# Kernel optimization log

Hardware: AMD Instinct MI355X
Metric: run time of the kernel (lower is better)

## Reference

```python
import jax, jax.numpy as jnp
import numpy as np

OBS_DIM, GOAL_DIM, NUM_SKILLS, ACTION_DIM = 256, 64, 16, 32
HIDDEN = 128
BATCH = 65536


def setup_inputs() -> dict:
    key = jax.random.key(0)
    ks = jax.random.split(key, 10)
    s = lambda k, shape, fan_in: jax.random.normal(k, shape, jnp.float32) * (1.0 / np.sqrt(fan_in))
    return {
        "obs": jax.random.normal(ks[0], (BATCH, OBS_DIM), jnp.float32),
        "goals": jax.random.normal(ks[1], (BATCH, GOAL_DIM), jnp.float32),
        # gate (AlphaNet) params
        "Wa1": s(ks[2], (OBS_DIM + GOAL_DIM, HIDDEN), OBS_DIM + GOAL_DIM),
        "ba1": jnp.zeros((HIDDEN,), jnp.float32),
        "Wa2": s(ks[3], (HIDDEN, NUM_SKILLS), HIDDEN),
        "ba2": jnp.zeros((NUM_SKILLS,), jnp.float32),
        # stacked executor params: [S, in, out]
        "W1": s(ks[4], (NUM_SKILLS, OBS_DIM, HIDDEN), OBS_DIM),
        "b1": jnp.zeros((NUM_SKILLS, HIDDEN), jnp.float32),
        "W2": s(ks[5], (NUM_SKILLS, HIDDEN, ACTION_DIM), HIDDEN),
        "b2": jnp.zeros((NUM_SKILLS, ACTION_DIM), jnp.float32),
    }


def reference(obs, goals, Wa1, ba1, Wa2, ba2, W1, b1, W2, b2):
    # gate: softmax(Linear(ReLU(Linear(cat(obs, goals)))))
    concat_input = jnp.concatenate([obs, goals], axis=-1)  # [B, O+G]
    ha = jax.nn.relu(concat_input @ Wa1 + ba1)             # [B, H]
    alphas = jax.nn.softmax(ha @ Wa2 + ba2, axis=-1)       # [B, S]

    # all experts as one grouped GEMM over stacked weights
    h = jax.nn.relu(jnp.einsum("bo,soh->bsh", obs, W1) + b1[None])  # [B, S, H]
    skill_outputs = jnp.einsum("bsh,sha->bsa", h, W2) + b2[None]    # [B, S, A]

    # weighted sum over skills
    mixed_action = jnp.einsum("bsa,bs->ba", skill_outputs, alphas)  # [B, A]
    return mixed_action, alphas
```

## Files before the change

kernel.cpp:

```cpp
#include <hip/hip_runtime.h>


typedef __attribute__((ext_vector_type(8))) short    bf16x8;
typedef __attribute__((ext_vector_type(4))) float    f32x4;
typedef __attribute__((ext_vector_type(4))) _Float16 f16x4;
using half2v = decltype(__builtin_amdgcn_cvt_pkrtz(0.f, 0.f));

#define GATE_W1_OFF   0
#define GATE_W2_OFF   81920
#define GATE_BYTES    86016
#define S_W1_STRIDE   528
#define S_W2_OFF      67584
#define S_W2_STRIDE   272
#define S_IMG         76288
#define SKILL_OFF     86016
#define LDS_BYTES     162304

__device__ __forceinline__ unsigned short f2bf(float f) {
  unsigned u = __builtin_bit_cast(unsigned, f);
  return (unsigned short)((u + 0x7FFFu + ((u >> 16) & 1u)) >> 16);
}

__device__ __forceinline__ bf16x8 pack_bf8(f32x4 a, f32x4 b) {
  bf16x8 r;
  r[0] = (short)f2bf(a[0]); r[1] = (short)f2bf(a[1]);
  r[2] = (short)f2bf(a[2]); r[3] = (short)f2bf(a[3]);
  r[4] = (short)f2bf(b[0]); r[5] = (short)f2bf(b[1]);
  r[6] = (short)f2bf(b[2]); r[7] = (short)f2bf(b[3]);
  return r;
}

#define RELU_SCALE_PACK(dst, v, av, z)                                   \
  {                                                                      \
    half2v lo_ = __builtin_amdgcn_cvt_pkrtz((v)[0], (v)[1]);             \
    half2v hi_ = __builtin_amdgcn_cvt_pkrtz((v)[2], (v)[3]);             \
    lo_ = __builtin_elementwise_max(lo_, z) * (av);                      \
    hi_ = __builtin_elementwise_max(hi_, z) * (av);                      \
    dst[0] = (_Float16)lo_[0]; dst[1] = (_Float16)lo_[1];                \
    dst[2] = (_Float16)hi_[0]; dst[3] = (_Float16)hi_[1];                \
  }

__global__ void prep_weights(const float* __restrict__ Wa1, const float* __restrict__ Wa2,
                             const float* __restrict__ W1,  const float* __restrict__ W2,
                             unsigned char* __restrict__ ws) {
  int i = blockIdx.x * 256 + threadIdx.x;
  if (i < 524288) {
    int s = i >> 15, r = i & 32767, h = r >> 8, o = r & 255;
    float v = W1[(s * 256 + o) * 128 + h];
    *(unsigned short*)(ws + SKILL_OFF + s * S_IMG + h * S_W1_STRIDE + 2 * o) = f2bf(v);
  } else if (i < 589824) {
    int j = i - 524288, s = j >> 12, r = j & 4095, a = r >> 7, h = r & 127;
    float v = W2[(s * 128 + h) * 32 + a];
    *(_Float16*)(ws + SKILL_OFF + s * S_IMG + S_W2_OFF + a * S_W2_STRIDE + 2 * h) =
        (_Float16)v;
  } else if (i < 630784) {
    int j = i - 589824, h = j / 320, o = j - h * 320;
    float v = Wa1[o * 128 + h];
    *(unsigned short*)(ws + GATE_W1_OFF + h * 640 +
                       ((2 * o) ^ ((h & 7) << 4))) = f2bf(v);
  } else if (i < 632832) {
    int j = i - 630784, n = j >> 7, h = j & 127;
    float v = Wa2[h * 16 + n];
    *(_Float16*)(ws + GATE_W2_OFF + n * 256 +
                 ((2 * h) ^ ((n & 7) << 3))) = (_Float16)v;
  }
}

__device__ __forceinline__ void stage_lin(const unsigned char* gsrc, unsigned char* ldst,
                                          int tid, int bytes) {
  for (int off = tid * 16; off < bytes; off += 256 * 16) {
    __builtin_amdgcn_global_load_lds(
        (const __attribute__((address_space(1))) unsigned int*)(const void*)(gsrc + off),
        (__attribute__((address_space(3))) unsigned int*)(void*)(ldst + off), 16, 0, 0);
  }
}

__global__ __launch_bounds__(256, 1)
void mop_fused(const float* __restrict__ obs, const float* __restrict__ goals,
               const float* __restrict__ ba1, const float* __restrict__ ba2,
               const float* __restrict__ b1,  const float* __restrict__ b2,
               const unsigned char* __restrict__ ws, float* __restrict__ dout) {
  extern __shared__ unsigned char smem[];
  const int tid  = threadIdx.x;
  const int lane = tid & 63;
  const int wave = tid >> 6;
  const int l15  = lane & 15;
  const int g    = lane >> 4;
  const int swz4 = (lane & 7) << 4;
  const int swz3 = (lane & 7) << 3;
  const int rowbase = blockIdx.x * 256 + wave * 64;

  float* out_mixed = dout;
  float* out_alpha = dout + 65536 * 32;

  const int lw1 = l15 * S_W1_STRIDE + 16 * g;
  const int lw2 = S_W2_OFF + l15 * S_W2_STRIDE + 8 * g;

  stage_lin(ws, smem, tid, GATE_BYTES);

  bf16x8 obsf[4][8];
  bf16x8 goalf[4][2];
  #pragma unroll
  for (int nb = 0; nb < 4; ++nb) {
    const float* rp = obs + (size_t)(rowbase + nb * 16 + l15) * 256 + 8 * g;
    #pragma unroll
    for (int t = 0; t < 8; ++t) {
      f32x4 a = *(const f32x4*)(rp + 32 * t);
      f32x4 c = *(const f32x4*)(rp + 32 * t + 4);
      obsf[nb][t] = pack_bf8(a, c);
    }
    const float* gp = goals + (size_t)(rowbase + nb * 16 + l15) * 64 + 8 * g;
    #pragma unroll
    for (int t = 0; t < 2; ++t) {
      f32x4 a = *(const f32x4*)(gp + 32 * t);
      f32x4 c = *(const f32x4*)(gp + 32 * t + 4);
      goalf[nb][t] = pack_bf8(a, c);
    }
  }

  __syncthreads();

  stage_lin(ws + SKILL_OFF, smem + GATE_BYTES, tid, S_IMG);

  f32x4 gacc[4][8];
  #pragma unroll
  for (int ht = 0; ht < 8; ++ht) {
    f32x4 bias = *(const f32x4*)(ba1 + 16 * ht + 4 * g);
    #pragma unroll
    for (int nb = 0; nb < 4; ++nb) gacc[nb][ht] = bias;
  }
  #pragma unroll
  for (int t = 0; t < 10; ++t) {
    bf16x8 bf[4];
    #pragma unroll
    for (int nb = 0; nb < 4; ++nb) bf[nb] = (t < 8) ? obsf[nb][t] : goalf[nb][t - 8];
    #pragma unroll
    for (int ht = 0; ht < 8; ++ht) {
      int row = 16 * ht + l15;
      bf16x8 af = *(const bf16x8*)(smem + GATE_W1_OFF + row * 640 +
                                   ((64 * t + 16 * g) ^ swz4));
      #pragma unroll
      for (int nb = 0; nb < 4; ++nb)
        gacc[nb][ht] = __builtin_amdgcn_mfma_f32_16x16x32_bf16(af, bf[nb], gacc[nb][ht], 0, 0, 0);
    }
  }

  const half2v zh = __builtin_amdgcn_cvt_pkrtz(0.f, 0.f);
  f32x4 alph[4];
  #pragma unroll
  for (int nb = 0; nb < 4; ++nb) {
    f32x4 lacc = *(const f32x4*)(ba2 + 4 * g);
    #pragma unroll
    for (int ht = 0; ht < 8; ++ht) {
      f32x4 v = gacc[nb][ht];
      f16x4 hf;
      {
        half2v lo_ = __builtin_amdgcn_cvt_pkrtz(v[0], v[1]);
        half2v hi_ = __builtin_amdgcn_cvt_pkrtz(v[2], v[3]);
        lo_ = __builtin_elementwise_max(lo_, zh);
        hi_ = __builtin_elementwise_max(hi_, zh);
        hf[0] = (_Float16)lo_[0]; hf[1] = (_Float16)lo_[1];
        hf[2] = (_Float16)hi_[0]; hf[3] = (_Float16)hi_[1];
      }
      f16x4 wf = *(const f16x4*)(smem + GATE_W2_OFF + l15 * 256 +
                                 ((32 * ht + 8 * g) ^ swz3));
      lacc = __builtin_amdgcn_mfma_f32_16x16x16f16(wf, hf, lacc, 0, 0, 0);
    }
    float m = fmaxf(fmaxf(lacc[0], lacc[1]), fmaxf(lacc[2], lacc[3]));
    m = fmaxf(m, __shfl_xor(m, 16, 64));
    m = fmaxf(m, __shfl_xor(m, 32, 64));
    f32x4 e;
    e[0] = __expf(lacc[0] - m); e[1] = __expf(lacc[1] - m);
    e[2] = __expf(lacc[2] - m); e[3] = __expf(lacc[3] - m);
    float ssum = e[0] + e[1] + e[2] + e[3];
    ssum += __shfl_xor(ssum, 16, 64);
    ssum += __shfl_xor(ssum, 32, 64);
    float inv = 1.0f / ssum;
    alph[nb] = e * inv;
    *(f32x4*)(out_alpha + (size_t)(rowbase + nb * 16 + l15) * 16 + 4 * g) = alph[nb];
  }

  __syncthreads();

  f32x4 macc[4][2] = {};
  for (int s = 0; s < 16; ++s) {
    const unsigned char* buf = smem + ((s & 1) ? 0 : GATE_BYTES);
    if (s < 15) {
      unsigned char* nbuf = smem + (((s + 1) & 1) ? 0 : GATE_BYTES);
      stage_lin(ws + SKILL_OFF + (size_t)(s + 1) * S_IMG, nbuf, tid, S_IMG);
    }
    const int asrc = ((s >> 2) << 4) | l15;
    float av[4];
    half2v ah[4];
    #pragma unroll
    for (int nb = 0; nb < 4; ++nb) {
      float c0 = (s & 1) ? alph[nb][1] : alph[nb][0];
      float c1 = (s & 1) ? alph[nb][3] : alph[nb][2];
      av[nb] = __shfl((s & 2) ? c1 : c0, asrc, 64);
      ah[nb] = __builtin_amdgcn_cvt_pkrtz(av[nb], av[nb]);
    }

    f32x4 b1v[8];
    #pragma unroll
    for (int ht = 0; ht < 8; ++ht)
      b1v[ht] = *(const f32x4*)(b1 + s * 128 + 16 * ht + 4 * g);
    f32x4 b2v[2];
    #pragma unroll
    for (int ta = 0; ta < 2; ++ta)
      b2v[ta] = *(const f32x4*)(b2 + s * 32 + 16 * ta + 4 * g);

    const unsigned char* w1p = buf + lw1;
    const unsigned char* w2p = buf + lw2;

    #pragma unroll
    for (int ht = 0; ht < 8; ++ht) {
      f32x4 acc[4];
      #pragma unroll
      for (int nb = 0; nb < 4; ++nb) acc[nb] = b1v[ht];
      #pragma unroll
      for (int t = 0; t < 8; ++t) {
        bf16x8 af = *(const bf16x8*)(w1p + ht * 8448 + t * 64);
        #pragma unroll
        for (int nb = 0; nb < 4; ++nb)
          acc[nb] = __builtin_amdgcn_mfma_f32_16x16x32_bf16(af, obsf[nb][t], acc[nb], 0, 0, 0);
      }
      f16x4 hf[4];
      #pragma unroll
      for (int nb = 0; nb < 4; ++nb) RELU_SCALE_PACK(hf[nb], acc[nb], ah[nb], zh);
      #pragma unroll
      for (int ta = 0; ta < 2; ++ta) {
        f16x4 wf = *(const f16x4*)(w2p + ta * 4352 + ht * 32);
        #pragma unroll
        for (int nb = 0; nb < 4; ++nb)
          macc[nb][ta] = __builtin_amdgcn_mfma_f32_16x16x16f16(wf, hf[nb], macc[nb][ta], 0, 0, 0);
      }
    }
    #pragma unroll
    for (int nb = 0; nb < 4; ++nb) {
      #pragma unroll
      for (int ta = 0; ta < 2; ++ta)
        macc[nb][ta] = macc[nb][ta] + b2v[ta] * av[nb];
    }
    __syncthreads();
  }

  #pragma unroll
  for (int nb = 0; nb < 4; ++nb) {
    #pragma unroll
    for (int ta = 0; ta < 2; ++ta) {
      *(f32x4*)(out_mixed + (size_t)(rowbase + nb * 16 + l15) * 32 + 16 * ta + 4 * g) =
          macc[nb][ta];
    }
  }
}

extern "C" void kernel_launch(void* const* d_in, const int* in_sizes, int n_in,
                              void* d_out, int out_size, void* d_ws, size_t ws_size,
                              hipStream_t stream) {
  const float* obs   = (const float*)d_in[0];
  const float* goals = (const float*)d_in[1];
  const float* Wa1   = (const float*)d_in[2];
  const float* ba1   = (const float*)d_in[3];
  const float* Wa2   = (const float*)d_in[4];
  const float* ba2   = (const float*)d_in[5];
  const float* W1    = (const float*)d_in[6];
  const float* b1    = (const float*)d_in[7];
  const float* W2    = (const float*)d_in[8];
  const float* b2    = (const float*)d_in[9];
  unsigned char* ws  = (unsigned char*)d_ws;
  float* out = (float*)d_out;

  prep_weights<<<2472, 256, 0, stream>>>(Wa1, Wa2, W1, W2, ws);
  mop_fused<<<256, 256, LDS_BYTES, stream>>>(obs, goals, ba1, ba2, b1, b2, ws, out);
}
```

Before: 113.9 us.

## Split hidden dimension across two wave groups per block with LDS reduction

Doubles the block to 512 threads. Each group of four waves handles half of the hidden units for the same 256 rows, in both the gate MLP and the skill executors. Partial gate logits and mixed-action accumulators are summed across the two halves through LDS. The biases move into the staged LDS weight images, bf16 packing now uses the hardware v_cvt_pk_bf16_f32 instruction, and MFMA loops get raised wave priority. The intent is more waves per CU to hide latency, at the cost of extra LDS reductions, barriers, and duplicated obs register loading in both halves.

```diff
diff --git a/kernel.cpp b/kernel.cpp
--- a/kernel.cpp
+++ b/kernel.cpp
@@ -8,13 +8,16 @@
 
 #define GATE_W1_OFF   0
 #define GATE_W2_OFF   81920
-#define GATE_BYTES    86016
+#define GATE_BA1_OFF  86016
+#define GATE_BA2_OFF  86528
+#define GATE_BYTES    86592
 #define S_W1_STRIDE   528
 #define S_W2_OFF      67584
 #define S_W2_STRIDE   272
-#define S_IMG         76288
-#define SKILL_OFF     86016
-#define LDS_BYTES     162304
+#define S_B1_OFF      76288
+#define S_B2_OFF      76800
+#define S_IMG         76928
+#define LDS_BYTES     163520
 
 __device__ __forceinline__ unsigned short f2bf(float f) {
   unsigned u = __builtin_bit_cast(unsigned, f);
@@ -22,12 +25,12 @@
 }
 
 __device__ __forceinline__ bf16x8 pack_bf8(f32x4 a, f32x4 b) {
-  bf16x8 r;
-  r[0] = (short)f2bf(a[0]); r[1] = (short)f2bf(a[1]);
-  r[2] = (short)f2bf(a[2]); r[3] = (short)f2bf(a[3]);
-  r[4] = (short)f2bf(b[0]); r[5] = (short)f2bf(b[1]);
-  r[6] = (short)f2bf(b[2]); r[7] = (short)f2bf(b[3]);
-  return r;
+  int4 r;
+  asm("v_cvt_pk_bf16_f32 %0, %1, %2" : "=v"(r.x) : "v"(a[0]), "v"(a[1]));
+  asm("v_cvt_pk_bf16_f32 %0, %1, %2" : "=v"(r.y) : "v"(a[2]), "v"(a[3]));
+  asm("v_cvt_pk_bf16_f32 %0, %1, %2" : "=v"(r.z) : "v"(b[0]), "v"(b[1]));
+  asm("v_cvt_pk_bf16_f32 %0, %1, %2" : "=v"(r.w) : "v"(b[2]), "v"(b[3]));
+  return __builtin_bit_cast(bf16x8, r);
 }
 
 #define RELU_SCALE_PACK(dst, v, av, z)                                   \
@@ -39,19 +42,30 @@
     dst[0] = (_Float16)lo_[0]; dst[1] = (_Float16)lo_[1];                \
     dst[2] = (_Float16)hi_[0]; dst[3] = (_Float16)hi_[1];                \
   }
+#define RELU_PACK(dst, v, z)                                             \
+  {                                                                      \
+    half2v lo_ = __builtin_amdgcn_cvt_pkrtz((v)[0], (v)[1]);             \
+    half2v hi_ = __builtin_amdgcn_cvt_pkrtz((v)[2], (v)[3]);             \
+    lo_ = __builtin_elementwise_max(lo_, z);                             \
+    hi_ = __builtin_elementwise_max(hi_, z);                             \
+    dst[0] = (_Float16)lo_[0]; dst[1] = (_Float16)lo_[1];                \
+    dst[2] = (_Float16)hi_[0]; dst[3] = (_Float16)hi_[1];                \
+  }
 
 __global__ void prep_weights(const float* __restrict__ Wa1, const float* __restrict__ Wa2,
+                             const float* __restrict__ ba1, const float* __restrict__ ba2,
                              const float* __restrict__ W1,  const float* __restrict__ W2,
+                             const float* __restrict__ b1,  const float* __restrict__ b2,
                              unsigned char* __restrict__ ws) {
   int i = blockIdx.x * 256 + threadIdx.x;
   if (i < 524288) {
     int s = i >> 15, r = i & 32767, h = r >> 8, o = r & 255;
     float v = W1[(s * 256 + o) * 128 + h];
-    *(unsigned short*)(ws + SKILL_OFF + s * S_IMG + h * S_W1_STRIDE + 2 * o) = f2bf(v);
+    *(unsigned short*)(ws + GATE_BYTES + s * S_IMG + h * S_W1_STRIDE + 2 * o) = f2bf(v);
   } else if (i < 589824) {
     int j = i - 524288, s = j >> 12, r = j & 4095, a = r >> 7, h = r & 127;
     float v = W2[(s * 128 + h) * 32 + a];
-    *(_Float16*)(ws + SKILL_OFF + s * S_IMG + S_W2_OFF + a * S_W2_STRIDE + 2 * h) =
+    *(_Float16*)(ws + GATE_BYTES + s * S_IMG + S_W2_OFF + a * S_W2_STRIDE + 2 * h) =
         (_Float16)v;
   } else if (i < 630784) {
     int j = i - 589824, h = j / 320, o = j - h * 320;
@@ -63,38 +77,52 @@
     float v = Wa2[h * 16 + n];
     *(_Float16*)(ws + GATE_W2_OFF + n * 256 +
                  ((2 * h) ^ ((n & 7) << 3))) = (_Float16)v;
+  } else if (i < 634880) {
+    int j = i - 632832, s = j >> 7, h = j & 127;
+    *(float*)(ws + GATE_BYTES + s * S_IMG + S_B1_OFF + 4 * h) = b1[s * 128 + h];
+  } else if (i < 635392) {
+    int j = i - 634880, s = j >> 5, a = j & 31;
+    *(float*)(ws + GATE_BYTES + s * S_IMG + S_B2_OFF + 4 * a) = b2[s * 32 + a];
+  } else if (i < 635520) {
+    int j = i - 635392;
+    *(float*)(ws + GATE_BA1_OFF + 4 * j) = ba1[j];
+  } else if (i < 635536) {
+    int j = i - 635520;
+    *(float*)(ws + GATE_BA2_OFF + 4 * j) = ba2[j];
   }
 }
 
 __device__ __forceinline__ void stage_lin(const unsigned char* gsrc, unsigned char* ldst,
                                           int tid, int bytes) {
-  for (int off = tid * 16; off < bytes; off += 256 * 16) {
+  for (int off = tid * 16; off < bytes; off += 512 * 16) {
     __builtin_amdgcn_global_load_lds(
         (const __attribute__((address_space(1))) unsigned int*)(const void*)(gsrc + off),
         (__attribute__((address_space(3))) unsigned int*)(void*)(ldst + off), 16, 0, 0);
   }
 }
 
-__global__ __launch_bounds__(256, 1)
+__global__ __launch_bounds__(512, 2)
 void mop_fused(const float* __restrict__ obs, const float* __restrict__ goals,
-               const float* __restrict__ ba1, const float* __restrict__ ba2,
-               const float* __restrict__ b1,  const float* __restrict__ b2,
                const unsigned char* __restrict__ ws, float* __restrict__ dout) {
   extern __shared__ unsigned char smem[];
   const int tid  = threadIdx.x;
   const int lane = tid & 63;
   const int wave = tid >> 6;
+  const int half = wave >> 2;
+  const int pr   = wave & 3;
   const int l15  = lane & 15;
   const int g    = lane >> 4;
   const int swz4 = (lane & 7) << 4;
   const int swz3 = (lane & 7) << 3;
-  const int rowbase = blockIdx.x * 256 + wave * 64;
+  const int rowbase = blockIdx.x * 256 + pr * 64;
 
   float* out_mixed = dout;
   float* out_alpha = dout + 65536 * 32;
 
-  const int lw1 = l15 * S_W1_STRIDE + 16 * g;
-  const int lw2 = S_W2_OFF + l15 * S_W2_STRIDE + 8 * g;
+  const int lw1 = half * 33792 + l15 * S_W1_STRIDE + 16 * g;
+  const int lw2 = S_W2_OFF + l15 * S_W2_STRIDE + 8 * g + half * 128;
+  const int lb1 = S_B1_OFF + 256 * half + 16 * g;
+  const int lb2 = S_B2_OFF + 16 * g;
 
   stage_lin(ws, smem, tid, GATE_BYTES);
 
@@ -120,12 +148,12 @@
 
   __syncthreads();
 
-  stage_lin(ws + SKILL_OFF, smem + GATE_BYTES, tid, S_IMG);
-
-  f32x4 gacc[4][8];
-  #pragma unroll
-  for (int ht = 0; ht < 8; ++ht) {
-    f32x4 bias = *(const f32x4*)(ba1 + 16 * ht + 4 * g);
+  stage_lin(ws + GATE_BYTES, smem + GATE_BYTES, tid, S_IMG);
+
+  f32x4 gacc[4][4];
+  #pragma unroll
+  for (int ht = 0; ht < 4; ++ht) {
+    f32x4 bias = *(const f32x4*)(smem + GATE_BA1_OFF + 256 * half + 64 * ht + 16 * g);
     #pragma unroll
     for (int nb = 0; nb < 4; ++nb) gacc[nb][ht] = bias;
   }
@@ -135,8 +163,8 @@
     #pragma unroll
     for (int nb = 0; nb < 4; ++nb) bf[nb] = (t < 8) ? obsf[nb][t] : goalf[nb][t - 8];
     #pragma unroll
-    for (int ht = 0; ht < 8; ++ht) {
-      int row = 16 * ht + l15;
+    for (int ht = 0; ht < 4; ++ht) {
+      int row = 64 * half + 16 * ht + l15;
       bf16x8 af = *(const bf16x8*)(smem + GATE_W1_OFF + row * 640 +
                                    ((64 * t + 16 * g) ^ swz4));
       #pragma unroll
@@ -146,38 +174,48 @@
   }
 
   const half2v zh = __builtin_amdgcn_cvt_pkrtz(0.f, 0.f);
+  f32x4 lacc[4];
+  #pragma unroll
+  for (int nb = 0; nb < 4; ++nb) {
+    lacc[nb] = (half == 0) ? *(const f32x4*)(smem + GATE_BA2_OFF + 16 * g)
+                           : f32x4{0.f, 0.f, 0.f, 0.f};
+    #pragma unroll
+    for (int ht = 0; ht < 4; ++ht) {
+      f16x4 hf;
+      RELU_PACK(hf, gacc[nb][ht], zh);
+      f16x4 wf = *(const f16x4*)(smem + GATE_W2_OFF + l15 * 256 +
+                                 ((32 * (4 * half + ht) + 8 * g) ^ swz3));
+      lacc[nb] = __builtin_amdgcn_mfma_f32_16x16x16f16(wf, hf, lacc[nb], 0, 0, 0);
+    }
+  }
+
+  __syncthreads();
+  #pragma unroll
+  for (int nb = 0; nb < 4; ++nb)
+    #pragma unroll
+    for (int r = 0; r < 4; ++r)
+      *(float*)(smem + wave * 4352 + nb * 1088 + (4 * g + r) * 68 + 4 * l15) = lacc[nb][r];
+  __syncthreads();
+
   f32x4 alph[4];
   #pragma unroll
   for (int nb = 0; nb < 4; ++nb) {
-    f32x4 lacc = *(const f32x4*)(ba2 + 4 * g);
-    #pragma unroll
-    for (int ht = 0; ht < 8; ++ht) {
-      f32x4 v = gacc[nb][ht];
-      f16x4 hf;
-      {
-        half2v lo_ = __builtin_amdgcn_cvt_pkrtz(v[0], v[1]);
-        half2v hi_ = __builtin_amdgcn_cvt_pkrtz(v[2], v[3]);
-        lo_ = __builtin_elementwise_max(lo_, zh);
-        hi_ = __builtin_elementwise_max(hi_, zh);
-        hf[0] = (_Float16)lo_[0]; hf[1] = (_Float16)lo_[1];
-        hf[2] = (_Float16)hi_[0]; hf[3] = (_Float16)hi_[1];
-      }
-      f16x4 wf = *(const f16x4*)(smem + GATE_W2_OFF + l15 * 256 +
-                                 ((32 * ht + 8 * g) ^ swz3));
-      lacc = __builtin_amdgcn_mfma_f32_16x16x16f16(wf, hf, lacc, 0, 0, 0);
-    }
-    float m = fmaxf(fmaxf(lacc[0], lacc[1]), fmaxf(lacc[2], lacc[3]));
+    f32x4 l = lacc[nb];
+    #pragma unroll
+    for (int r = 0; r < 4; ++r)
+      l[r] += *(const float*)(smem + (wave ^ 4) * 4352 + nb * 1088 + (4 * g + r) * 68 + 4 * l15);
+    float m = fmaxf(fmaxf(l[0], l[1]), fmaxf(l[2], l[3]));
     m = fmaxf(m, __shfl_xor(m, 16, 64));
     m = fmaxf(m, __shfl_xor(m, 32, 64));
     f32x4 e;
-    e[0] = __expf(lacc[0] - m); e[1] = __expf(lacc[1] - m);
-    e[2] = __expf(lacc[2] - m); e[3] = __expf(lacc[3] - m);
+    e[0] = __expf(l[0] - m); e[1] = __expf(l[1] - m);
+    e[2] = __expf(l[2] - m); e[3] = __expf(l[3] - m);
     float ssum = e[0] + e[1] + e[2] + e[3];
     ssum += __shfl_xor(ssum, 16, 64);
     ssum += __shfl_xor(ssum, 32, 64);
-    float inv = 1.0f / ssum;
-    alph[nb] = e * inv;
-    *(f32x4*)(out_alpha + (size_t)(rowbase + nb * 16 + l15) * 16 + 4 * g) = alph[nb];
+    alph[nb] = e * (1.0f / ssum);
+    if (half == 0)
+      *(f32x4*)(out_alpha + (size_t)(rowbase + nb * 16 + l15) * 16 + 4 * g) = alph[nb];
   }
 
   __syncthreads();
@@ -187,8 +225,17 @@
     const unsigned char* buf = smem + ((s & 1) ? 0 : GATE_BYTES);
     if (s < 15) {
       unsigned char* nbuf = smem + (((s + 1) & 1) ? 0 : GATE_BYTES);
-      stage_lin(ws + SKILL_OFF + (size_t)(s + 1) * S_IMG, nbuf, tid, S_IMG);
-    }
+      stage_lin(ws + GATE_BYTES + (size_t)(s + 1) * S_IMG, nbuf, tid, S_IMG);
+    }
+    f32x4 b1v[4];
+    #pragma unroll
+    for (int ht = 0; ht < 4; ++ht)
+      b1v[ht] = *(const f32x4*)(buf + lb1 + 64 * ht);
+    f32x4 b2v[2];
+    #pragma unroll
+    for (int ta = 0; ta < 2; ++ta)
+      b2v[ta] = *(const f32x4*)(buf + lb2 + 64 * ta);
+
     const int asrc = ((s >> 2) << 4) | l15;
     float av[4];
     half2v ah[4];
@@ -200,20 +247,12 @@
       ah[nb] = __builtin_amdgcn_cvt_pkrtz(av[nb], av[nb]);
     }
 
-    f32x4 b1v[8];
-    #pragma unroll
-    for (int ht = 0; ht < 8; ++ht)
-      b1v[ht] = *(const f32x4*)(b1 + s * 128 + 16 * ht + 4 * g);
-    f32x4 b2v[2];
-    #pragma unroll
-    for (int ta = 0; ta < 2; ++ta)
-      b2v[ta] = *(const f32x4*)(b2 + s * 32 + 16 * ta + 4 * g);
-
     const unsigned char* w1p = buf + lw1;
     const unsigned char* w2p = buf + lw2;
 
-    #pragma unroll
-    for (int ht = 0; ht < 8; ++ht) {
+    __builtin_amdgcn_s_setprio(1);
+    #pragma unroll
+    for (int ht = 0; ht < 4; ++ht) {
       f32x4 acc[4];
       #pragma unroll
       for (int nb = 0; nb < 4; ++nb) acc[nb] = b1v[ht];
@@ -235,21 +274,37 @@
           macc[nb][ta] = __builtin_amdgcn_mfma_f32_16x16x16f16(wf, hf[nb], macc[nb][ta], 0, 0, 0);
       }
     }
-    #pragma unroll
-    for (int nb = 0; nb < 4; ++nb) {
-      #pragma unroll
-      for (int ta = 0; ta < 2; ++ta)
-        macc[nb][ta] = macc[nb][ta] + b2v[ta] * av[nb];
+    __builtin_amdgcn_s_setprio(0);
+    if (half == 0) {
+      #pragma unroll
+      for (int nb = 0; nb < 4; ++nb)
+        #pragma unroll
+        for (int ta = 0; ta < 2; ++ta)
+          macc[nb][ta] = macc[nb][ta] + b2v[ta] * av[nb];
     }
     __syncthreads();
   }
 
   #pragma unroll
-  for (int nb = 0; nb < 4; ++nb) {
+  for (int nb = 0; nb < 4; ++nb)
+    #pragma unroll
+    for (int ta = 0; ta < 2; ++ta)
+      #pragma unroll
+      for (int r = 0; r < 4; ++r)
+        *(float*)(smem + wave * 8704 + nb * 2176 + (16 * ta + 4 * g + r) * 68 + 4 * l15) =
+            macc[nb][ta][r];
+  __syncthreads();
+  #pragma unroll
+  for (int j = 0; j < 2; ++j) {
+    const int nb = 2 * half + j;
     #pragma unroll
     for (int ta = 0; ta < 2; ++ta) {
-      *(f32x4*)(out_mixed + (size_t)(rowbase + nb * 16 + l15) * 32 + 16 * ta + 4 * g) =
-          macc[nb][ta];
+      f32x4 v = macc[nb][ta];
+      #pragma unroll
+      for (int r = 0; r < 4; ++r)
+        v[r] += *(const float*)(smem + (wave ^ 4) * 8704 + nb * 2176 +
+                                (16 * ta + 4 * g + r) * 68 + 4 * l15);
+      *(f32x4*)(out_mixed + (size_t)(rowbase + nb * 16 + l15) * 32 + 16 * ta + 4 * g) = v;
     }
   }
 }
@@ -270,6 +325,6 @@
   unsigned char* ws  = (unsigned char*)d_ws;
   float* out = (float*)d_out;
 
-  prep_weights<<<2472, 256, 0, stream>>>(Wa1, Wa2, W1, W2, ws);
-  mop_fused<<<256, 256, LDS_BYTES, stream>>>(obs, goals, ba1, ba2, b1, b2, ws, out);
-}
+  prep_weights<<<2483, 256, 0, stream>>>(Wa1, Wa2, ba1, ba2, W1, W2, b1, b2, ws);
+  mop_fused<<<256, 512, LDS_BYTES, stream>>>(obs, goals, ws, out);
+}
```

Measured after the change: 108.4 us. -4.9%, faster.
